# Performance work log

Hardware: AMD Instinct MI355X
Metric: run time of the kernel (lower is better)

## Reference

```python
import jax, jax.numpy as jnp
import numpy as np

ALPHA = 0.2  # LeakyReLU negative slope
N_NODES = 50000
N_EDGES = 800000
IN_F = 128
OUT_F = 64


def setup_inputs() -> dict:
    key = jax.random.key(0)
    k1, k2, k3, k4 = jax.random.split(key, 4)
    x = jax.random.normal(k1, (N_NODES, IN_F), dtype=jnp.float32)
    edge_index = jax.random.randint(k2, (2, N_EDGES), 0, N_NODES, dtype=jnp.int64)
    # xavier_uniform-ish scales
    W = jax.random.uniform(k3, (IN_F, OUT_F), dtype=jnp.float32,
                           minval=-1.0, maxval=1.0) * (1.414 * np.sqrt(6.0 / (IN_F + OUT_F)))
    a = jax.random.uniform(k4, (2 * OUT_F, 1), dtype=jnp.float32,
                           minval=-1.0, maxval=1.0) * (1.414 * np.sqrt(6.0 / (2 * OUT_F + 1)))
    return {"x": x, "edge_index": edge_index, "W": W, "a": a}


def reference(x, edge_index, W, a):
    Wh = x @ W                               # [N, F_out]
    src = edge_index[0]
    dst = edge_index[1]
    Wh_src = Wh[src]                         # [E, F_out] gather
    Wh_dst = Wh[dst]                         # [E, F_out] gather
    # concat([Wh_src, Wh_dst]) @ a == Wh_src @ a_top + Wh_dst @ a_bot
    F_out = Wh.shape[1]
    a_top = a[:F_out, 0]
    a_bot = a[F_out:, 0]
    e = jax.nn.leaky_relu(Wh_src @ a_top + Wh_dst @ a_bot, negative_slope=ALPHA)  # [E]
    # NOTE: original normalizes softmax over ALL edges (dim=0), not per node.
    attention = jax.nn.softmax(e)            # [E]
    # dropout skipped (eval mode, deterministic reference)
    msgs = Wh_dst * attention[:, None]       # [E, F_out]
    h_prime = jax.ops.segment_sum(msgs, src, num_segments=Wh.shape[0])  # scatter-add
    return jax.nn.elu(h_prime)
```

## Files before the change

kernel.cpp:

```cpp
#include <hip/hip_runtime.h>
#include <math.h>

#define N_NODES 50000
#define N_EDGES 800000
#define IN_F 128
#define OUT_F 64
#define LRELU_ALPHA 0.2f

#define NPB 64
#define NBUCK ((N_NODES + NPB - 1) / NPB)
#define EPT 16
#define NBT ((N_EDGES / EPT + 255) / 256)
#define CHUNK 2048

typedef __attribute__((ext_vector_type(8))) short bf16x8;
typedef __attribute__((ext_vector_type(4))) float f32x4;

__device__ inline float wred_sum(float v) {
#pragma unroll
    for (int o = 32; o > 0; o >>= 1) v += __shfl_down(v, o, 64);
    return v;
}

__device__ inline unsigned bf16r(float f) {
    unsigned u = __float_as_uint(f);
    u += 0x7fffu + ((u >> 16) & 1u);
    return u >> 16;
}

__global__ __launch_bounds__(1024) void k_proj(const float* __restrict__ W,
                                               const float* __restrict__ a,
                                               float* __restrict__ wt,
                                               float* __restrict__ wb,
                                               unsigned short* __restrict__ Wtb,
                                               int* __restrict__ bcnt) {
    int k = threadIdx.x;
    if (k < NBUCK) bcnt[k] = 0;
    if (k >= 128) return;
    float s = 0.0f, t = 0.0f;
#pragma unroll
    for (int c4 = 0; c4 < 64; c4 += 4) {
        float4 wv = *reinterpret_cast<const float4*>(W + k * 64 + c4);
        float4 at = *reinterpret_cast<const float4*>(a + c4);
        float4 ab = *reinterpret_cast<const float4*>(a + 64 + c4);
        s = fmaf(wv.w, at.w, fmaf(wv.z, at.z, fmaf(wv.y, at.y, fmaf(wv.x, at.x, s))));
        t = fmaf(wv.w, ab.w, fmaf(wv.z, ab.z, fmaf(wv.y, ab.y, fmaf(wv.x, ab.x, t))));
        Wtb[(c4 + 0) * 128 + k] = (unsigned short)bf16r(wv.x);
        Wtb[(c4 + 1) * 128 + k] = (unsigned short)bf16r(wv.y);
        Wtb[(c4 + 2) * 128 + k] = (unsigned short)bf16r(wv.z);
        Wtb[(c4 + 3) * 128 + k] = (unsigned short)bf16r(wv.w);
    }
    wt[k] = s;
    wb[k] = t;
}

__global__ __launch_bounds__(256, 4) void k_wh(const float* __restrict__ x,
                                               const unsigned short* __restrict__ Wtb,
                                               const float* __restrict__ wt,
                                               const float* __restrict__ wb,
                                               const int* __restrict__ src,
                                               unsigned short* __restrict__ Whb,
                                               float* __restrict__ sv,
                                               float* __restrict__ tv,
                                               int* __restrict__ bcnt) {
    __shared__ unsigned short xb[64 * 128];
    __shared__ unsigned short wtl[64 * 128];
    __shared__ int hc[NBUCK];

    const int tid = threadIdx.x;
    const int row0 = blockIdx.x * 64;

    for (int i = tid; i < NBUCK; i += 256) hc[i] = 0;

    for (int ci = tid; ci < 1024; ci += 256) {
        int c = ci >> 4, kb = ci & 15;
        int4 v = *reinterpret_cast<const int4*>(Wtb + ci * 8);
        *reinterpret_cast<int4*>(&wtl[c * 128 + (kb ^ (c & 15)) * 8]) = v;
    }

    const int cc = (tid & 31) << 2;
    float4 wt4 = *reinterpret_cast<const float4*>(wt + cc);
    float4 wb4 = *reinterpret_cast<const float4*>(wb + cc);
    float ps[8], pt[8];
#pragma unroll
    for (int it = 0; it < 8; ++it) {
        int i = tid + it * 256;
        int rl = i >> 5;
        int r = row0 + rl;
        float4 v = make_float4(0.f, 0.f, 0.f, 0.f);
        if (r < N_NODES) v = *reinterpret_cast<const float4*>(x + (size_t)r * IN_F + cc);
        ps[it] = fmaf(v.w, wt4.w, fmaf(v.z, wt4.z, fmaf(v.y, wt4.y, v.x * wt4.x)));
        pt[it] = fmaf(v.w, wb4.w, fmaf(v.z, wb4.z, fmaf(v.y, wb4.y, v.x * wb4.x)));
        int kb = cc >> 3;
        uint2 pk;
        pk.x = bf16r(v.x) | (bf16r(v.y) << 16);
        pk.y = bf16r(v.z) | (bf16r(v.w) << 16);
        *reinterpret_cast<uint2*>(
            &xb[rl * 128 + (kb ^ (rl & 15)) * 8 + ((cc >> 2) & 1) * 4]) = pk;
    }

    {
        int j0 = blockIdx.x * 1024 + tid * 4;
        if (j0 < N_EDGES) {
            int4 s4 = *reinterpret_cast<const int4*>(src + j0);
            atomicAdd(&hc[s4.x >> 6], 1);
            atomicAdd(&hc[s4.y >> 6], 1);
            atomicAdd(&hc[s4.z >> 6], 1);
            atomicAdd(&hc[s4.w >> 6], 1);
        }
    }
    __syncthreads();

    const int l = tid & 63, w = tid >> 6;
    const int rloc0 = w * 16;
    const int arow = rloc0 + (l & 15);
    const int kgrp = l >> 4;
    f32x4 acc[4] = {f32x4{0,0,0,0}, f32x4{0,0,0,0}, f32x4{0,0,0,0}, f32x4{0,0,0,0}};
#pragma unroll
    for (int t = 0; t < 4; ++t) {
        int kb = t * 4 + kgrp;
        bf16x8 af = *reinterpret_cast<const bf16x8*>(
            &xb[arow * 128 + (kb ^ (arow & 15)) * 8]);
#pragma unroll
        for (int ct = 0; ct < 4; ++ct) {
            int brow = ct * 16 + (l & 15);
            bf16x8 bfr = *reinterpret_cast<const bf16x8*>(
                &wtl[brow * 128 + (kb ^ (brow & 15)) * 8]);
            acc[ct] = __builtin_amdgcn_mfma_f32_16x16x32_bf16(af, bfr, acc[ct], 0, 0, 0);
        }
    }

#pragma unroll
    for (int ct = 0; ct < 4; ++ct) {
#pragma unroll
        for (int i = 0; i < 4; ++i) {
            int r = row0 + rloc0 + (l >> 4) * 4 + i;
            if (r < N_NODES)
                Whb[(size_t)r * OUT_F + ct * 16 + (l & 15)] =
                    (unsigned short)bf16r(acc[ct][i]);
        }
    }

#pragma unroll
    for (int it = 0; it < 8; ++it) {
        float s = ps[it], t2 = pt[it];
#pragma unroll
        for (int o = 1; o < 32; o <<= 1) {
            s += __shfl_xor(s, o, 64);
            t2 += __shfl_xor(t2, o, 64);
        }
        int r = row0 + (tid >> 5) + it * 8;
        if ((tid & 31) == 0 && r < N_NODES) { sv[r] = s; tv[r] = t2; }
    }

    __syncthreads();
    for (int i = tid; i < NBUCK; i += 256) {
        int v = hc[i];
        if (v) atomicAdd(&bcnt[i], v);
    }
}

__global__ __launch_bounds__(1024) void k_bscan(const int* __restrict__ bcnt,
                                                int* __restrict__ bbase,
                                                int* __restrict__ cursor) {
    __shared__ int s[1024];
    int t = threadIdx.x;
    int c = (t < NBUCK) ? bcnt[t] : 0;
    s[t] = c;
    __syncthreads();
#pragma unroll
    for (int o = 1; o < 1024; o <<= 1) {
        int v = (t >= o) ? s[t - o] : 0;
        __syncthreads();
        s[t] += v;
        __syncthreads();
    }
    if (t < NBUCK) {
        int ex = s[t] - c;
        bbase[t] = ex;
        cursor[t] = ex;
    }
    if (t == 0) bbase[NBUCK] = N_EDGES;
}

__global__ __launch_bounds__(256) void k_binscatter(const int* __restrict__ src,
                                                    const int* __restrict__ dst,
                                                    const float* __restrict__ sv,
                                                    const float* __restrict__ tv,
                                                    int* __restrict__ cursor,
                                                    int2* __restrict__ rec,
                                                    float* __restrict__ psum) {
    __shared__ int lcnt[NBUCK];
    __shared__ int lbase[NBUCK];
    const int tid = threadIdx.x;
    for (int i = tid; i < NBUCK; i += 256) lcnt[i] = 0;
    __syncthreads();

    int t = blockIdx.x * 256 + tid;
    int j0 = t * EPT;
    bool ok = (j0 < N_EDGES);

    int s_[EPT], d_[EPT], rk[EPT];
    float ev[EPT];
    float lsum = 0.0f;
    if (ok) {
#pragma unroll
        for (int q = 0; q < 4; q++) {
            int4 s4 = *reinterpret_cast<const int4*>(src + j0 + q * 4);
            int4 d4 = *reinterpret_cast<const int4*>(dst + j0 + q * 4);
            s_[q * 4 + 0] = s4.x; s_[q * 4 + 1] = s4.y;
            s_[q * 4 + 2] = s4.z; s_[q * 4 + 3] = s4.w;
            d_[q * 4 + 0] = d4.x; d_[q * 4 + 1] = d4.y;
            d_[q * 4 + 2] = d4.z; d_[q * 4 + 3] = d4.w;
        }
        float svv[EPT], tvv[EPT];
#pragma unroll
        for (int k = 0; k < EPT; k++) svv[k] = sv[s_[k]];
#pragma unroll
        for (int k = 0; k < EPT; k++) tvv[k] = tv[d_[k]];
#pragma unroll
        for (int k = 0; k < EPT; k++) {
            float vv = svv[k] + tvv[k];
            vv = vv > 0.0f ? vv : LRELU_ALPHA * vv;
            float e = __expf(vv);
            ev[k] = e;
            lsum += e;
        }
#pragma unroll
        for (int k = 0; k < EPT; k++) rk[k] = atomicAdd(&lcnt[s_[k] >> 6], 1);
    }
    __syncthreads();

    for (int i = tid; i < NBUCK; i += 256) {
        int c = lcnt[i];
        lbase[i] = c ? atomicAdd(&cursor[i], c) : 0;
    }
    __syncthreads();

    if (ok) {
#pragma unroll
        for (int k = 0; k < EPT; k++) {
            int b = s_[k] >> 6;
            rec[lbase[b] + rk[k]] =
                make_int2(d_[k] | ((s_[k] & (NPB - 1)) << 16), __float_as_int(ev[k]));
        }
    }

    float wsum = wred_sum(lsum);
    __shared__ float rsm[4];
    if ((tid & 63) == 0) rsm[tid >> 6] = wsum;
    __syncthreads();
    if (tid == 0)
        psum[blockIdx.x] = rsm[0] + rsm[1] + rsm[2] + rsm[3];
}

__global__ __launch_bounds__(256) void k_rsum(const float* __restrict__ psum,
                                              int n, float* __restrict__ g) {
    __shared__ float red[4];
    int t = threadIdx.x;
    float lsum = 0.0f;
    for (int i = t; i < n; i += 256) lsum += psum[i];
    float ws = wred_sum(lsum);
    if ((t & 63) == 0) red[t >> 6] = ws;
    __syncthreads();
    if (t == 0) g[0] = 1.0f / (red[0] + red[1] + red[2] + red[3]);
}

__global__ __launch_bounds__(512) void k_bgather(const int* __restrict__ bbase,
                                                 const int2* __restrict__ rec,
                                                 const float* __restrict__ g,
                                                 const unsigned short* __restrict__ Whb,
                                                 float* __restrict__ out) {
    __shared__ int2 sorted[CHUNK];
    __shared__ int scnt[NPB], soff[NPB], shead[NPB];

    const int tid = threadIdx.x;
    const int lane = tid & 63, w = tid >> 6;
    const int j = lane & 31, h = lane >> 5;
    const int b = blockIdx.x;
    const float ginv = g[0];
    const int e0 = bbase[b], e1 = bbase[b + 1];

    float ax[8], ay[8];
#pragma unroll
    for (int k = 0; k < 8; k++) { ax[k] = 0.0f; ay[k] = 0.0f; }

    for (int base = e0; base < e1; base += CHUNK) {
        int m = e1 - base;
        if (m > CHUNK) m = CHUNK;

        int2 rr[4];
        int ln[4];
        bool vv[4];
        if (tid < NPB) scnt[tid] = 0;
        __syncthreads();
#pragma unroll
        for (int q = 0; q < 4; q++) {
            int idx = tid + q * 512;
            vv[q] = idx < m;
            rr[q] = make_int2(0, 0);
            ln[q] = 0;
            if (vv[q]) {
                rr[q] = rec[base + idx];
                ln[q] = (rr[q].x >> 16) & (NPB - 1);
                atomicAdd(&scnt[ln[q]], 1);
            }
        }
        __syncthreads();

        if (tid < 64) {
            int c = scnt[tid];
            int run = c;
#pragma unroll
            for (int o = 1; o < 64; o <<= 1) {
                int src_ln = (tid >= o) ? (tid - o) : tid;
                int t2 = __shfl(run, src_ln, 64);
                if (tid >= o) run += t2;
            }
            int excl = run - c;
            soff[tid] = excl;
            shead[tid] = excl;
        }
        __syncthreads();

#pragma unroll
        for (int q = 0; q < 4; q++) {
            if (vv[q]) {
                int pos = atomicAdd(&shead[ln[q]], 1);
                sorted[pos] = make_int2(rr[q].x & 0xFFFF, rr[q].y);
            }
        }
        __syncthreads();

#pragma unroll
        for (int k = 0; k < 8; k++) {
            int node = w * 8 + k;
            int lo = soff[node], c = scnt[node];
            float px = 0.0f, py = 0.0f;
            int i = 0;
            for (; i + 7 < c; i += 8) {
                int2 q0 = sorted[lo + i + h];
                int2 q1 = sorted[lo + i + 2 + h];
                int2 q2 = sorted[lo + i + 4 + h];
                int2 q3 = sorted[lo + i + 6 + h];
                const unsigned* p0 =
                    reinterpret_cast<const unsigned*>(Whb + (size_t)q0.x * OUT_F);
                const unsigned* p1 =
                    reinterpret_cast<const unsigned*>(Whb + (size_t)q1.x * OUT_F);
                const unsigned* p2 =
                    reinterpret_cast<const unsigned*>(Whb + (size_t)q2.x * OUT_F);
                const unsigned* p3 =
                    reinterpret_cast<const unsigned*>(Whb + (size_t)q3.x * OUT_F);
                unsigned u0 = p0[j];
                unsigned u1 = p1[j];
                unsigned u2 = p2[j];
                unsigned u3 = p3[j];
                float att0 = __int_as_float(q0.y);
                float att1 = __int_as_float(q1.y);
                float att2 = __int_as_float(q2.y);
                float att3 = __int_as_float(q3.y);
                px = fmaf(att0, __uint_as_float((u0 & 0xffffu) << 16), px);
                py = fmaf(att0, __uint_as_float(u0 & 0xffff0000u), py);
                px = fmaf(att1, __uint_as_float((u1 & 0xffffu) << 16), px);
                py = fmaf(att1, __uint_as_float(u1 & 0xffff0000u), py);
                px = fmaf(att2, __uint_as_float((u2 & 0xffffu) << 16), px);
                py = fmaf(att2, __uint_as_float(u2 & 0xffff0000u), py);
                px = fmaf(att3, __uint_as_float((u3 & 0xffffu) << 16), px);
                py = fmaf(att3, __uint_as_float(u3 & 0xffff0000u), py);
            }
            for (; i < c; i += 2) {
                int ii = i + h;
                bool val = ii < c;
                int2 q = sorted[lo + (val ? ii : i)];
                const unsigned* p =
                    reinterpret_cast<const unsigned*>(Whb + (size_t)q.x * OUT_F);
                unsigned u = p[j];
                float att = val ? __int_as_float(q.y) : 0.0f;
                px = fmaf(att, __uint_as_float((u & 0xffffu) << 16), px);
                py = fmaf(att, __uint_as_float(u & 0xffff0000u), py);
            }
            ax[k] += px;
            ay[k] += py;
        }
        __syncthreads();
    }

#pragma unroll
    for (int k = 0; k < 8; k++) {
        float sx = ax[k] + __shfl_down(ax[k], 32, 64);
        float sy = ay[k] + __shfl_down(ay[k], 32, 64);
        int n = b * NPB + w * 8 + k;
        if (h == 0 && n < N_NODES) {
            float2 v;
            v.x = sx * ginv;
            v.y = sy * ginv;
            v.x = v.x > 0.0f ? v.x : expm1f(v.x);
            v.y = v.y > 0.0f ? v.y : expm1f(v.y);
            *reinterpret_cast<float2*>(out + (size_t)n * OUT_F + 2 * j) = v;
        }
    }
}

extern "C" void kernel_launch(void* const* d_in, const int* in_sizes, int n_in,
                              void* d_out, int out_size, void* d_ws, size_t ws_size,
                              hipStream_t stream) {
    const float* x  = (const float*)d_in[0];
    const int*   ei = (const int*)d_in[1];
    const float* W  = (const float*)d_in[2];
    const float* a  = (const float*)d_in[3];
    float* out = (float*)d_out;

    const int* src = ei;
    const int* dst = ei + N_EDGES;

    unsigned short* Whb = (unsigned short*)d_ws;
    float* sv     = (float*)(Whb + (size_t)N_NODES * OUT_F);
    float* tv     = sv + N_NODES;
    float* psum   = tv + N_NODES;
    float* g      = psum + 512;
    float* wt     = g + 2;
    float* wb     = wt + 128;
    int*   bcnt   = (int*)(wb + 128);
    int*   bbase  = bcnt + NBUCK;
    int*   cursor = bbase + NBUCK + 1;
    size_t used = (size_t)((char*)(cursor + NBUCK) - (char*)d_ws);
    used = (used + 15) & ~(size_t)15;
    unsigned short* Wtb = (unsigned short*)((char*)d_ws + used);
    used += 8192 * sizeof(unsigned short);
    used = (used + 15) & ~(size_t)15;
    int2*  rec  = (int2*)((char*)d_ws + used);

    k_proj<<<1, 1024, 0, stream>>>(W, a, wt, wb, Wtb, bcnt);
    k_wh<<<(N_NODES + 63) / 64, 256, 0, stream>>>(x, Wtb, wt, wb, src, Whb, sv, tv, bcnt);
    k_bscan<<<1, 1024, 0, stream>>>(bcnt, bbase, cursor);
    k_binscatter<<<NBT, 256, 0, stream>>>(src, dst, sv, tv, cursor, rec, psum);
    k_rsum<<<1, 256, 0, stream>>>(psum, NBT, g);
    k_bgather<<<NBUCK, 512, 0, stream>>>(bbase, rec, g, Whb, out);
}
```

Before: 103.0 us.

## Fold projection and global-sum kernels into neighbours, use warp-shuffle bucket scan

```diff
diff --git a/kernel.cpp b/kernel.cpp
--- a/kernel.cpp
+++ b/kernel.cpp
@@ -28,36 +28,9 @@
     return u >> 16;
 }
 
-__global__ __launch_bounds__(1024) void k_proj(const float* __restrict__ W,
+__global__ __launch_bounds__(256, 4) void k_wh(const float* __restrict__ x,
+                                               const float* __restrict__ W,
                                                const float* __restrict__ a,
-                                               float* __restrict__ wt,
-                                               float* __restrict__ wb,
-                                               unsigned short* __restrict__ Wtb,
-                                               int* __restrict__ bcnt) {
-    int k = threadIdx.x;
-    if (k < NBUCK) bcnt[k] = 0;
-    if (k >= 128) return;
-    float s = 0.0f, t = 0.0f;
-#pragma unroll
-    for (int c4 = 0; c4 < 64; c4 += 4) {
-        float4 wv = *reinterpret_cast<const float4*>(W + k * 64 + c4);
-        float4 at = *reinterpret_cast<const float4*>(a + c4);
-        float4 ab = *reinterpret_cast<const float4*>(a + 64 + c4);
-        s = fmaf(wv.w, at.w, fmaf(wv.z, at.z, fmaf(wv.y, at.y, fmaf(wv.x, at.x, s))));
-        t = fmaf(wv.w, ab.w, fmaf(wv.z, ab.z, fmaf(wv.y, ab.y, fmaf(wv.x, ab.x, t))));
-        Wtb[(c4 + 0) * 128 + k] = (unsigned short)bf16r(wv.x);
-        Wtb[(c4 + 1) * 128 + k] = (unsigned short)bf16r(wv.y);
-        Wtb[(c4 + 2) * 128 + k] = (unsigned short)bf16r(wv.z);
-        Wtb[(c4 + 3) * 128 + k] = (unsigned short)bf16r(wv.w);
-    }
-    wt[k] = s;
-    wb[k] = t;
-}
-
-__global__ __launch_bounds__(256, 4) void k_wh(const float* __restrict__ x,
-                                               const unsigned short* __restrict__ Wtb,
-                                               const float* __restrict__ wt,
-                                               const float* __restrict__ wb,
                                                const int* __restrict__ src,
                                                unsigned short* __restrict__ Whb,
                                                float* __restrict__ sv,
@@ -65,6 +38,7 @@
                                                int* __restrict__ bcnt) {
     __shared__ unsigned short xb[64 * 128];
     __shared__ unsigned short wtl[64 * 128];
+    __shared__ float wt_s[128], wb_s[128];
     __shared__ int hc[NBUCK];
 
     const int tid = threadIdx.x;
@@ -72,15 +46,46 @@
 
     for (int i = tid; i < NBUCK; i += 256) hc[i] = 0;
 
-    for (int ci = tid; ci < 1024; ci += 256) {
-        int c = ci >> 4, kb = ci & 15;
-        int4 v = *reinterpret_cast<const int4*>(Wtb + ci * 8);
-        *reinterpret_cast<int4*>(&wtl[c * 128 + (kb ^ (c & 15)) * 8]) = v;
-    }
+    for (int i = tid; i < 2048; i += 256) {
+        int k = i >> 4, c4 = (i & 15) << 2;
+        float4 wv = *reinterpret_cast<const float4*>(W + k * 64 + c4);
+        int kb = k >> 3, kr = k & 7;
+        wtl[(c4 + 0) * 128 + ((kb ^ ((c4 + 0) & 15)) << 3) + kr] = (unsigned short)bf16r(wv.x);
+        wtl[(c4 + 1) * 128 + ((kb ^ ((c4 + 1) & 15)) << 3) + kr] = (unsigned short)bf16r(wv.y);
+        wtl[(c4 + 2) * 128 + ((kb ^ ((c4 + 2) & 15)) << 3) + kr] = (unsigned short)bf16r(wv.z);
+        wtl[(c4 + 3) * 128 + ((kb ^ ((c4 + 3) & 15)) << 3) + kr] = (unsigned short)bf16r(wv.w);
+    }
+
+    if (tid < 128) {
+        int k = tid;
+        float s = 0.0f, t = 0.0f;
+#pragma unroll
+        for (int c4 = 0; c4 < 64; c4 += 4) {
+            float4 wv = *reinterpret_cast<const float4*>(W + k * 64 + c4);
+            float4 at = *reinterpret_cast<const float4*>(a + c4);
+            float4 ab = *reinterpret_cast<const float4*>(a + 64 + c4);
+            s = fmaf(wv.w, at.w, fmaf(wv.z, at.z, fmaf(wv.y, at.y, fmaf(wv.x, at.x, s))));
+            t = fmaf(wv.w, ab.w, fmaf(wv.z, ab.z, fmaf(wv.y, ab.y, fmaf(wv.x, ab.x, t))));
+        }
+        wt_s[k] = s;
+        wb_s[k] = t;
+    }
+
+    {
+        int j0 = blockIdx.x * 1024 + tid * 4;
+        if (j0 < N_EDGES) {
+            int4 s4 = *reinterpret_cast<const int4*>(src + j0);
+            atomicAdd(&hc[s4.x >> 6], 1);
+            atomicAdd(&hc[s4.y >> 6], 1);
+            atomicAdd(&hc[s4.z >> 6], 1);
+            atomicAdd(&hc[s4.w >> 6], 1);
+        }
+    }
+    __syncthreads();
 
     const int cc = (tid & 31) << 2;
-    float4 wt4 = *reinterpret_cast<const float4*>(wt + cc);
-    float4 wb4 = *reinterpret_cast<const float4*>(wb + cc);
+    float4 wt4 = *reinterpret_cast<const float4*>(wt_s + cc);
+    float4 wb4 = *reinterpret_cast<const float4*>(wb_s + cc);
     float ps[8], pt[8];
 #pragma unroll
     for (int it = 0; it < 8; ++it) {
@@ -98,17 +103,6 @@
         *reinterpret_cast<uint2*>(
             &xb[rl * 128 + (kb ^ (rl & 15)) * 8 + ((cc >> 2) & 1) * 4]) = pk;
     }
-
-    {
-        int j0 = blockIdx.x * 1024 + tid * 4;
-        if (j0 < N_EDGES) {
-            int4 s4 = *reinterpret_cast<const int4*>(src + j0);
-            atomicAdd(&hc[s4.x >> 6], 1);
-            atomicAdd(&hc[s4.y >> 6], 1);
-            atomicAdd(&hc[s4.z >> 6], 1);
-            atomicAdd(&hc[s4.w >> 6], 1);
-        }
-    }
     __syncthreads();
 
     const int l = tid & 63, w = tid >> 6;
@@ -153,7 +147,6 @@
         if ((tid & 31) == 0 && r < N_NODES) { sv[r] = s; tv[r] = t2; }
     }
 
-    __syncthreads();
     for (int i = tid; i < NBUCK; i += 256) {
         int v = hc[i];
         if (v) atomicAdd(&bcnt[i], v);
@@ -163,20 +156,25 @@
 __global__ __launch_bounds__(1024) void k_bscan(const int* __restrict__ bcnt,
                                                 int* __restrict__ bbase,
                                                 int* __restrict__ cursor) {
-    __shared__ int s[1024];
-    int t = threadIdx.x;
+    __shared__ int wsum[16], woff[16];
+    int t = threadIdx.x, lane = t & 63, w = t >> 6;
     int c = (t < NBUCK) ? bcnt[t] : 0;
-    s[t] = c;
-    __syncthreads();
-#pragma unroll
-    for (int o = 1; o < 1024; o <<= 1) {
-        int v = (t >= o) ? s[t - o] : 0;
-        __syncthreads();
-        s[t] += v;
-        __syncthreads();
-    }
+    int run = c;
+#pragma unroll
+    for (int o = 1; o < 64; o <<= 1) {
+        int v = __shfl_up(run, o, 64);
+        if (lane >= o) run += v;
+    }
+    if (lane == 63) wsum[w] = run;
+    __syncthreads();
+    if (t == 0) {
+        int r = 0;
+#pragma unroll
+        for (int i = 0; i < 16; i++) { woff[i] = r; r += wsum[i]; }
+    }
+    __syncthreads();
+    int ex = run - c + woff[w];
     if (t < NBUCK) {
-        int ex = s[t] - c;
         bbase[t] = ex;
         cursor[t] = ex;
     }
@@ -254,32 +252,29 @@
         psum[blockIdx.x] = rsm[0] + rsm[1] + rsm[2] + rsm[3];
 }
 
-__global__ __launch_bounds__(256) void k_rsum(const float* __restrict__ psum,
-                                              int n, float* __restrict__ g) {
-    __shared__ float red[4];
-    int t = threadIdx.x;
-    float lsum = 0.0f;
-    for (int i = t; i < n; i += 256) lsum += psum[i];
-    float ws = wred_sum(lsum);
-    if ((t & 63) == 0) red[t >> 6] = ws;
-    __syncthreads();
-    if (t == 0) g[0] = 1.0f / (red[0] + red[1] + red[2] + red[3]);
-}
-
 __global__ __launch_bounds__(512) void k_bgather(const int* __restrict__ bbase,
                                                  const int2* __restrict__ rec,
-                                                 const float* __restrict__ g,
+                                                 const float* __restrict__ psum,
                                                  const unsigned short* __restrict__ Whb,
                                                  float* __restrict__ out) {
     __shared__ int2 sorted[CHUNK];
     __shared__ int scnt[NPB], soff[NPB], shead[NPB];
+    __shared__ float ginv_s;
 
     const int tid = threadIdx.x;
     const int lane = tid & 63, w = tid >> 6;
     const int j = lane & 31, h = lane >> 5;
     const int b = blockIdx.x;
-    const float ginv = g[0];
     const int e0 = bbase[b], e1 = bbase[b + 1];
+
+    if (tid < 64) {
+        float lsum = 0.0f;
+        for (int i = tid; i < NBT; i += 64) lsum += psum[i];
+        float ws = wred_sum(lsum);
+        if (tid == 0) ginv_s = 1.0f / ws;
+    }
+    __syncthreads();
+    const float ginv = ginv_s;
 
     float ax[8], ay[8];
 #pragma unroll
@@ -417,23 +412,16 @@
     float* sv     = (float*)(Whb + (size_t)N_NODES * OUT_F);
     float* tv     = sv + N_NODES;
     float* psum   = tv + N_NODES;
-    float* g      = psum + 512;
-    float* wt     = g + 2;
-    float* wb     = wt + 128;
-    int*   bcnt   = (int*)(wb + 128);
+    int*   bcnt   = (int*)(psum + 512);
     int*   bbase  = bcnt + NBUCK;
     int*   cursor = bbase + NBUCK + 1;
     size_t used = (size_t)((char*)(cursor + NBUCK) - (char*)d_ws);
     used = (used + 15) & ~(size_t)15;
-    unsigned short* Wtb = (unsigned short*)((char*)d_ws + used);
-    used += 8192 * sizeof(unsigned short);
-    used = (used + 15) & ~(size_t)15;
     int2*  rec  = (int2*)((char*)d_ws + used);
 
-    k_proj<<<1, 1024, 0, stream>>>(W, a, wt, wb, Wtb, bcnt);
-    k_wh<<<(N_NODES + 63) / 64, 256, 0, stream>>>(x, Wtb, wt, wb, src, Whb, sv, tv, bcnt);
+    hipMemsetAsync(bcnt, 0, NBUCK * sizeof(int), stream);
+    k_wh<<<(N_NODES + 63) / 64, 256, 0, stream>>>(x, W, a, src, Whb, sv, tv, bcnt);
     k_bscan<<<1, 1024, 0, stream>>>(bcnt, bbase, cursor);
     k_binscatter<<<NBT, 256, 0, stream>>>(src, dst, sv, tv, cursor, rec, psum);
-    k_rsum<<<1, 256, 0, stream>>>(psum, NBT, g);
-    k_bgather<<<NBUCK, 512, 0, stream>>>(bbase, rec, g, Whb, out);
-}
+    k_bgather<<<NBUCK, 512, 0, stream>>>(bbase, rec, psum, Whb, out);
+}
```

After: 102.2 us. About the same (-0.7%).
